# Performance work log

Hardware: AMD Instinct MI355X
Metric: run time of the kernel (lower is better)

The kernel has to match this reference:

```python
import jax, jax.numpy as jnp
import numpy as np

NX, DX, H, DO = 8192, 8, 1024, 1


def setup_inputs() -> dict:
    key = jax.random.key(0)
    ks = jax.random.split(key, 7)
    s1 = 1.0 / np.sqrt(DX)  # torch Linear default init bound
    s2 = 1.0 / np.sqrt(H)
    x = jax.random.normal(ks[0], (NX, DX), jnp.float32)
    W1 = jax.random.uniform(ks[1], (H, DX), jnp.float32, -s1, s1)
    b1 = jax.random.uniform(ks[2], (H,), jnp.float32, -s1, s1)
    W2 = jax.random.uniform(ks[3], (H, H), jnp.float32, -s2, s2)
    b2 = jax.random.uniform(ks[4], (H,), jnp.float32, -s2, s2)
    W3 = jax.random.uniform(ks[5], (DO, H), jnp.float32, -s2, s2)
    b3 = jax.random.uniform(ks[6], (DO,), jnp.float32, -s2, s2)
    return {"x": x, "W1": W1, "b1": b1, "W2": W2, "b2": b2, "W3": W3, "b3": b3}


def reference(x, W1, b1, W2, b2, W3, b3):
    # Forward: Linear -> Tanh -> Linear -> Tanh -> Linear
    z1 = jnp.tanh(x @ W1.T + b1)          # [nx, h]
    z2 = jnp.tanh(z1 @ W2.T + b2)         # [nx, h]
    y = z2 @ W3.T + b3                    # [nx, out]

    # DerivTanh(h) = 4/(e^-h + e^h)^2 = sech^2(h) = 1 - tanh(h)^2
    d1 = 1.0 - z1 * z1                    # [nx, h]
    d2 = 1.0 - z2 * z2                    # [nx, h]

    # Vectorized analytic Jacobian (original loops over each input dim k):
    # tmp_k = d2 * (W2 @ (d1 * W1[:, k]))  then  dydx_k = W3 @ tmp_k
    J = d1[:, :, None] * W1[None, :, :]                    # [nx, h, dx]
    J = d2[:, :, None] * jnp.einsum('ij,njk->nik', W2, J)  # [nx, h, dx]
    dydx = jnp.einsum('oj,njk->nok', W3, J)                # [nx, out, dx]
    # Match original list-of-dx ordering: dydx[k] has shape [nx, out]
    dydx = jnp.transpose(dydx, (2, 0, 1))                  # [dx, nx, out]
    return y, dydx
```

## Files before the change

kernel.cpp:

```cpp
#include <hip/hip_runtime.h>
#include <stdint.h>

#define NXS 8192
#define HS  1024

typedef __attribute__((ext_vector_type(8))) short short8;
typedef __attribute__((ext_vector_type(4))) float f32x4;

__device__ __forceinline__ float bf2f(uint32_t b) {
    union { uint32_t u; float f; } c; c.u = b << 16; return c.f;
}
__device__ __forceinline__ uint16_t f2bf(float f) {
    union { float f; uint32_t u; } c; c.f = f;
    return (uint16_t)((c.u + 0x7fffu + ((c.u >> 16) & 1u)) >> 16);
}
__device__ __forceinline__ void async_cp16(const void* g, void* l) {
    __builtin_amdgcn_global_load_lds(
        (const __attribute__((address_space(1))) void*)g,
        (__attribute__((address_space(3))) void*)l,
        16, 0, 0);
}

__global__ __launch_bounds__(256) void k01(
    const float* __restrict__ x, const float* __restrict__ W1,
    const float* __restrict__ b1, const float* __restrict__ W2,
    const float* __restrict__ b3, uint16_t* __restrict__ Z1,
    uint16_t* __restrict__ W2c, uint16_t* __restrict__ W2T,
    uint16_t* __restrict__ W1T, float* __restrict__ out)
{
    __shared__ float xs[8][8];
    __shared__ uint16_t tile[64][65];
    const int b = blockIdx.x;
    const int t = threadIdx.x;
    if (b < 1024) {
        const int n0 = b * 8;
        if (t < 64) xs[t >> 3][t & 7] = x[n0 * 8 + t];
        const int j = t * 4;
        float w[4][8];
#pragma unroll
        for (int c = 0; c < 4; ++c) {
            float4 w0 = *(const float4*)(W1 + (j + c) * 8);
            float4 w1 = *(const float4*)(W1 + (j + c) * 8 + 4);
            w[c][0] = w0.x; w[c][1] = w0.y; w[c][2] = w0.z; w[c][3] = w0.w;
            w[c][4] = w1.x; w[c][5] = w1.y; w[c][6] = w1.z; w[c][7] = w1.w;
        }
        float4 bb = *(const float4*)(b1 + j);
        const float bv[4] = {bb.x, bb.y, bb.z, bb.w};
        __syncthreads();
#pragma unroll
        for (int s = 0; s < 8; ++s) {
            ushort4 o;
            uint16_t* op = (uint16_t*)&o;
#pragma unroll
            for (int c = 0; c < 4; ++c) {
                float sum = bv[c];
#pragma unroll
                for (int k = 0; k < 8; ++k) sum += xs[s][k] * w[c][k];
                op[c] = f2bf(tanhf(sum));
            }
            *(ushort4*)(Z1 + (size_t)(n0 + s) * HS + j) = o;
        }
    } else if (b < 1280) {
        const int bb2 = b - 1024;
        const int bx = bb2 & 15, by = bb2 >> 4;
        const int tx = t & 63, ty = t >> 6;
#pragma unroll
        for (int rr = 0; rr < 64; rr += 4) {
            int r = ty + rr;
            uint16_t v = f2bf(W2[(size_t)(by * 64 + r) * HS + bx * 64 + tx]);
            W2c[(size_t)(by * 64 + r) * HS + bx * 64 + tx] = v;
            tile[r][tx] = v;
        }
        __syncthreads();
#pragma unroll
        for (int rr = 0; rr < 64; rr += 4)
            W2T[(size_t)(bx * 64 + ty + rr) * HS + by * 64 + tx] = tile[tx][ty + rr];
    } else if (b < 1568) {
        const int idx = (b - 1280) * 256 + t;
        out[idx] = (idx < NXS) ? b3[0] : 0.f;
    } else {
        const int idx = (b - 1568) * 256 + t;
        const int r = idx >> 10, c = idx & 1023;
        W1T[idx] = (r < 8) ? f2bf(W1[c * 8 + r]) : (uint16_t)0;
    }
}

template <int MODE>
__global__ __launch_bounds__(256, 4) void gemm_k(
    const uint16_t* __restrict__ A, const uint16_t* __restrict__ B,
    const float* __restrict__ bias, const float* __restrict__ W3,
    uint16_t* __restrict__ Out, float* __restrict__ yOut,
    const uint16_t* __restrict__ Z1, const uint16_t* __restrict__ W1T,
    float* __restrict__ dOut)
{
    __shared__ __attribute__((aligned(16))) uint16_t smem[12288];
    const int t = threadIdx.x;
    const int wave = t >> 6, lane = t & 63;
    const int lq = lane >> 4, lr = lane & 15;
    const int wm = wave >> 1, wn = wave & 1;
    const int rowBase = blockIdx.x * 64;
    const int colBase = blockIdx.y * 128;

    const int rA = t >> 2, qA = (t & 3) ^ (rA & 3);
    const int sB0 = t, sB1 = 256 + t;
    const int rB0 = sB0 >> 2, qB0 = (sB0 & 3) ^ (rB0 & 3);
    const int rB1 = sB1 >> 2, qB1 = (sB1 & 3) ^ (rB1 & 3);
    const uint16_t* gA  = A + (size_t)(rowBase + rA) * HS + qA * 8;
    const uint16_t* gB0 = B + (size_t)(colBase + rB0) * HS + qB0 * 8;
    const uint16_t* gB1 = B + (size_t)(colBase + rB1) * HS + qB1 * 8;

    f32x4 acc[2][4] = {};

    async_cp16(gA,  (char*)smem + t * 16);
    async_cp16(gB0, (char*)smem + 8192 + sB0 * 16);
    async_cp16(gB1, (char*)smem + 8192 + sB1 * 16);
    __syncthreads();

    int buf = 0;
    for (int k0 = 0; k0 < HS; k0 += 32, buf ^= 1) {
        if (k0 + 32 < HS) {
            const int ko = k0 + 32;
            async_cp16(gA + ko,  (char*)smem + (buf ^ 1) * 4096 + t * 16);
            async_cp16(gB0 + ko, (char*)smem + 8192 + (buf ^ 1) * 8192 + sB0 * 16);
            async_cp16(gB1 + ko, (char*)smem + 8192 + (buf ^ 1) * 8192 + sB1 * 16);
        }
        const short* pA = (const short*)smem + buf * 2048;
        const short* pB = (const short*)smem + 4096 + buf * 4096;
        short8 af[2], bfr[4];
#pragma unroll
        for (int ti = 0; ti < 2; ++ti) {
            int ar = wm * 32 + ti * 16 + lr;
            af[ti] = *(const short8*)(pA + ar * 32 + ((lq ^ (ar & 3)) << 3));
        }
#pragma unroll
        for (int tj = 0; tj < 4; ++tj) {
            int br = wn * 64 + tj * 16 + lr;
            bfr[tj] = *(const short8*)(pB + br * 32 + ((lq ^ (br & 3)) << 3));
        }
#pragma unroll
        for (int ti = 0; ti < 2; ++ti)
#pragma unroll
            for (int tj = 0; tj < 4; ++tj)
                acc[ti][tj] = __builtin_amdgcn_mfma_f32_16x16x32_bf16(
                    af[ti], bfr[tj], acc[ti][tj], 0, 0, 0);
        __syncthreads();
    }

    if (MODE == 0) {
        float cB[4], cW[4]; int cCol[4];
#pragma unroll
        for (int tj = 0; tj < 4; ++tj) {
            cCol[tj] = colBase + wn * 64 + tj * 16 + lr;
            cB[tj] = bias[cCol[tj]];
            cW[tj] = W3[cCol[tj]];
        }
#pragma unroll
        for (int ti = 0; ti < 2; ++ti) {
#pragma unroll
            for (int r = 0; r < 4; ++r) {
                int row = rowBase + wm * 32 + ti * 16 + lq * 4 + r;
                float ys = 0.f;
#pragma unroll
                for (int tj = 0; tj < 4; ++tj) {
                    float z2 = tanhf(acc[ti][tj][r] + cB[tj]);
                    ys += z2 * cW[tj];
                    Out[(size_t)row * HS + cCol[tj]] = f2bf((1.f - z2 * z2) * cW[tj]);
                }
                ys += __shfl_xor(ys, 1); ys += __shfl_xor(ys, 2);
                ys += __shfl_xor(ys, 4); ys += __shfl_xor(ys, 8);
                if (lr == 0) atomicAdd(&yOut[row], ys);
            }
        }
    } else {
#pragma unroll
        for (int ti = 0; ti < 2; ++ti)
#pragma unroll
            for (int r = 0; r < 4; ++r) {
                int rowl = wm * 32 + ti * 16 + lq * 4 + r;
                const size_t zrow = (size_t)(rowBase + rowl) * HS + colBase;
#pragma unroll
                for (int tj = 0; tj < 4; ++tj) {
                    int coll = wn * 64 + tj * 16 + lr;
                    float z1 = bf2f(Z1[zrow + coll]);
                    smem[rowl * 136 + coll] =
                        f2bf(acc[ti][tj][r] * (1.f - z1 * z1));
                }
            }
        __syncthreads();
        f32x4 dd = {};
#pragma unroll
        for (int kb = 0; kb < 4; ++kb) {
            short8 aF = *(const short8*)(smem + (wave * 16 + lr) * 136
                                         + kb * 32 + lq * 8);
            short8 bF = *(const short8*)(W1T + lr * HS + colBase
                                         + kb * 32 + lq * 8);
            dd = __builtin_amdgcn_mfma_f32_16x16x32_bf16(aF, bF, dd, 0, 0, 0);
        }
        if (lr < 8) {
            int row = rowBase + wave * 16 + lq * 4;
#pragma unroll
            for (int rg = 0; rg < 4; ++rg)
                atomicAdd(&dOut[(size_t)lr * NXS + row + rg], dd[rg]);
        }
    }
}

extern "C" void kernel_launch(void* const* d_in, const int* in_sizes, int n_in,
                              void* d_out, int out_size, void* d_ws, size_t ws_size,
                              hipStream_t stream) {
    (void)in_sizes; (void)n_in; (void)out_size; (void)ws_size;
    const float* x  = (const float*)d_in[0];
    const float* W1 = (const float*)d_in[1];
    const float* b1 = (const float*)d_in[2];
    const float* W2 = (const float*)d_in[3];
    const float* b2 = (const float*)d_in[4];
    const float* W3 = (const float*)d_in[5];
    const float* b3 = (const float*)d_in[6];
    float* out = (float*)d_out;

    char* ws = (char*)d_ws;
    uint16_t* Z1  = (uint16_t*)(ws);
    uint16_t* V   = (uint16_t*)(ws + (size_t)16 * 1024 * 1024);
    uint16_t* W2c = (uint16_t*)(ws + (size_t)32 * 1024 * 1024);
    uint16_t* W2T = (uint16_t*)(ws + (size_t)34 * 1024 * 1024);
    uint16_t* W1T = (uint16_t*)(ws + (size_t)36 * 1024 * 1024);

    k01<<<1632, 256, 0, stream>>>(x, W1, b1, W2, b3, Z1, W2c, W2T, W1T, out);
    gemm_k<0><<<dim3(NXS / 64, HS / 128), 256, 0, stream>>>(
        Z1, W2c, b2, W3, V, out, nullptr, nullptr, nullptr);
    gemm_k<1><<<dim3(NXS / 64, HS / 128), 256, 0, stream>>>(
        V, W2T, nullptr, nullptr, nullptr, nullptr, Z1, W1T, out + NXS);
}
```

Measured before the change: 147.2 us.

## Pre-pack W2 into MFMA fragment layout and load B operands directly into registers

The prep kernel now writes W2 and its transpose as bf16 in an MFMA-fragment-ordered layout, so each lane's 16-byte B fragment is contiguous. The GEMMs stop staging B through LDS and load these fragments straight from global memory into registers, prefetching one k-step ahead. Each wave now owns all 64 rows and 32 columns instead of a 2x2 wave grid. This removes the B tile's LDS traffic and shrinks LDS use, in exchange for more global/L2 loads of B per block, since each wave fetches its own columns.

```diff
diff --git a/kernel.cpp b/kernel.cpp
--- a/kernel.cpp
+++ b/kernel.cpp
@@ -25,13 +25,11 @@
     const float* __restrict__ x, const float* __restrict__ W1,
     const float* __restrict__ b1, const float* __restrict__ W2,
     const float* __restrict__ b3, uint16_t* __restrict__ Z1,
-    uint16_t* __restrict__ W2c, uint16_t* __restrict__ W2T,
+    uint16_t* __restrict__ Bp1, uint16_t* __restrict__ Bp2,
     uint16_t* __restrict__ W1T, float* __restrict__ out)
 {
     __shared__ float xs[8][8];
-    __shared__ uint16_t tile[64][65];
-    const int b = blockIdx.x;
-    const int t = threadIdx.x;
+    const int b = blockIdx.x, t = threadIdx.x;
     if (b < 1024) {
         const int n0 = b * 8;
         if (t < 64) xs[t >> 3][t & 7] = x[n0 * 8 + t];
@@ -60,34 +58,41 @@
             }
             *(ushort4*)(Z1 + (size_t)(n0 + s) * HS + j) = o;
         }
-    } else if (b < 1280) {
-        const int bb2 = b - 1024;
-        const int bx = bb2 & 15, by = bb2 >> 4;
-        const int tx = t & 63, ty = t >> 6;
-#pragma unroll
-        for (int rr = 0; rr < 64; rr += 4) {
-            int r = ty + rr;
-            uint16_t v = f2bf(W2[(size_t)(by * 64 + r) * HS + bx * 64 + tx]);
-            W2c[(size_t)(by * 64 + r) * HS + bx * 64 + tx] = v;
-            tile[r][tx] = v;
-        }
-        __syncthreads();
-#pragma unroll
-        for (int rr = 0; rr < 64; rr += 4)
-            W2T[(size_t)(bx * 64 + ty + rr) * HS + by * 64 + tx] = tile[tx][ty + rr];
-    } else if (b < 1568) {
-        const int idx = (b - 1280) * 256 + t;
+    } else if (b < 1536) {
+        const int tid = (b - 1024) * 256 + t;
+        const int l = tid & 63, c = (tid >> 6) & 31, g = tid >> 11;
+        const int lr = l & 15, lq = l >> 4;
+        const float* src = W2 + (size_t)(g * 16 + lr) * HS + c * 32 + lq * 8;
+        float4 a0 = *(const float4*)src;
+        float4 a1 = *(const float4*)(src + 4);
+        uint16_t o[8];
+        o[0] = f2bf(a0.x); o[1] = f2bf(a0.y); o[2] = f2bf(a0.z); o[3] = f2bf(a0.w);
+        o[4] = f2bf(a1.x); o[5] = f2bf(a1.y); o[6] = f2bf(a1.z); o[7] = f2bf(a1.w);
+        *(ushort4*)(Bp1 + (size_t)tid * 8)     = *(ushort4*)&o[0];
+        *(ushort4*)(Bp1 + (size_t)tid * 8 + 4) = *(ushort4*)&o[4];
+    } else if (b < 2048) {
+        const int tid = (b - 1536) * 256 + t;
+        const int l = tid & 63, c = (tid >> 6) & 31, g = tid >> 11;
+        const int lr = l & 15, lq = l >> 4;
+        uint16_t o[8];
+#pragma unroll
+        for (int j2 = 0; j2 < 8; ++j2)
+            o[j2] = f2bf(W2[(size_t)(c * 32 + lq * 8 + j2) * HS + g * 16 + lr]);
+        *(ushort4*)(Bp2 + (size_t)tid * 8)     = *(ushort4*)&o[0];
+        *(ushort4*)(Bp2 + (size_t)tid * 8 + 4) = *(ushort4*)&o[4];
+    } else if (b < 2336) {
+        const int idx = (b - 2048) * 256 + t;
         out[idx] = (idx < NXS) ? b3[0] : 0.f;
     } else {
-        const int idx = (b - 1568) * 256 + t;
-        const int r = idx >> 10, c = idx & 1023;
-        W1T[idx] = (r < 8) ? f2bf(W1[c * 8 + r]) : (uint16_t)0;
+        const int idx = (b - 2336) * 256 + t;
+        const int r = idx >> 10, cc = idx & 1023;
+        W1T[idx] = (r < 8) ? f2bf(W1[cc * 8 + r]) : (uint16_t)0;
     }
 }
 
 template <int MODE>
 __global__ __launch_bounds__(256, 4) void gemm_k(
-    const uint16_t* __restrict__ A, const uint16_t* __restrict__ B,
+    const uint16_t* __restrict__ A, const uint16_t* __restrict__ Bp,
     const float* __restrict__ bias, const float* __restrict__ W3,
     uint16_t* __restrict__ Out, float* __restrict__ yOut,
     const uint16_t* __restrict__ Z1, const uint16_t* __restrict__ W1T,
@@ -97,71 +102,62 @@
     const int t = threadIdx.x;
     const int wave = t >> 6, lane = t & 63;
     const int lq = lane >> 4, lr = lane & 15;
-    const int wm = wave >> 1, wn = wave & 1;
     const int rowBase = blockIdx.x * 64;
     const int colBase = blockIdx.y * 128;
 
     const int rA = t >> 2, qA = (t & 3) ^ (rA & 3);
-    const int sB0 = t, sB1 = 256 + t;
-    const int rB0 = sB0 >> 2, qB0 = (sB0 & 3) ^ (rB0 & 3);
-    const int rB1 = sB1 >> 2, qB1 = (sB1 & 3) ^ (rB1 & 3);
-    const uint16_t* gA  = A + (size_t)(rowBase + rA) * HS + qA * 8;
-    const uint16_t* gB0 = B + (size_t)(colBase + rB0) * HS + qB0 * 8;
-    const uint16_t* gB1 = B + (size_t)(colBase + rB1) * HS + qB1 * 8;
-
-    f32x4 acc[2][4] = {};
-
-    async_cp16(gA,  (char*)smem + t * 16);
-    async_cp16(gB0, (char*)smem + 8192 + sB0 * 16);
-    async_cp16(gB1, (char*)smem + 8192 + sB1 * 16);
+    const uint16_t* gA = A + (size_t)(rowBase + rA) * HS + qA * 8;
+
+    const uint16_t* pB0 = Bp + ((size_t)(colBase >> 4) + wave * 2) * 16384 + (size_t)lane * 8;
+    const uint16_t* pB1 = pB0 + 16384;
+
+    f32x4 acc[4][2] = {};
+
+    async_cp16(gA, (char*)smem + t * 16);
+    short8 b0 = *(const short8*)pB0;
+    short8 b1 = *(const short8*)pB1;
     __syncthreads();
 
     int buf = 0;
-    for (int k0 = 0; k0 < HS; k0 += 32, buf ^= 1) {
-        if (k0 + 32 < HS) {
-            const int ko = k0 + 32;
-            async_cp16(gA + ko,  (char*)smem + (buf ^ 1) * 4096 + t * 16);
-            async_cp16(gB0 + ko, (char*)smem + 8192 + (buf ^ 1) * 8192 + sB0 * 16);
-            async_cp16(gB1 + ko, (char*)smem + 8192 + (buf ^ 1) * 8192 + sB1 * 16);
+    for (int c = 0; c < 32; ++c, buf ^= 1) {
+        short8 b0n = b0, b1n = b1;
+        if (c < 31) {
+            async_cp16(gA + (c + 1) * 32, (char*)smem + (buf ^ 1) * 4096 + t * 16);
+            b0n = *(const short8*)(pB0 + (c + 1) * 512);
+            b1n = *(const short8*)(pB1 + (c + 1) * 512);
         }
         const short* pA = (const short*)smem + buf * 2048;
-        const short* pB = (const short*)smem + 4096 + buf * 4096;
-        short8 af[2], bfr[4];
-#pragma unroll
-        for (int ti = 0; ti < 2; ++ti) {
-            int ar = wm * 32 + ti * 16 + lr;
+        short8 af[4];
+#pragma unroll
+        for (int ti = 0; ti < 4; ++ti) {
+            int ar = ti * 16 + lr;
             af[ti] = *(const short8*)(pA + ar * 32 + ((lq ^ (ar & 3)) << 3));
         }
 #pragma unroll
-        for (int tj = 0; tj < 4; ++tj) {
-            int br = wn * 64 + tj * 16 + lr;
-            bfr[tj] = *(const short8*)(pB + br * 32 + ((lq ^ (br & 3)) << 3));
-        }
-#pragma unroll
-        for (int ti = 0; ti < 2; ++ti)
-#pragma unroll
-            for (int tj = 0; tj < 4; ++tj)
-                acc[ti][tj] = __builtin_amdgcn_mfma_f32_16x16x32_bf16(
-                    af[ti], bfr[tj], acc[ti][tj], 0, 0, 0);
+        for (int ti = 0; ti < 4; ++ti) {
+            acc[ti][0] = __builtin_amdgcn_mfma_f32_16x16x32_bf16(af[ti], b0, acc[ti][0], 0, 0, 0);
+            acc[ti][1] = __builtin_amdgcn_mfma_f32_16x16x32_bf16(af[ti], b1, acc[ti][1], 0, 0, 0);
+        }
         __syncthreads();
+        b0 = b0n; b1 = b1n;
     }
 
     if (MODE == 0) {
-        float cB[4], cW[4]; int cCol[4];
-#pragma unroll
-        for (int tj = 0; tj < 4; ++tj) {
-            cCol[tj] = colBase + wn * 64 + tj * 16 + lr;
+        float cB[2], cW[2]; int cCol[2];
+#pragma unroll
+        for (int tj = 0; tj < 2; ++tj) {
+            cCol[tj] = colBase + wave * 32 + tj * 16 + lr;
             cB[tj] = bias[cCol[tj]];
             cW[tj] = W3[cCol[tj]];
         }
 #pragma unroll
-        for (int ti = 0; ti < 2; ++ti) {
+        for (int ti = 0; ti < 4; ++ti) {
 #pragma unroll
             for (int r = 0; r < 4; ++r) {
-                int row = rowBase + wm * 32 + ti * 16 + lq * 4 + r;
+                int row = rowBase + ti * 16 + lq * 4 + r;
                 float ys = 0.f;
 #pragma unroll
-                for (int tj = 0; tj < 4; ++tj) {
+                for (int tj = 0; tj < 2; ++tj) {
                     float z2 = tanhf(acc[ti][tj][r] + cB[tj]);
                     ys += z2 * cW[tj];
                     Out[(size_t)row * HS + cCol[tj]] = f2bf((1.f - z2 * z2) * cW[tj]);
@@ -173,14 +169,14 @@
         }
     } else {
 #pragma unroll
-        for (int ti = 0; ti < 2; ++ti)
+        for (int ti = 0; ti < 4; ++ti)
 #pragma unroll
             for (int r = 0; r < 4; ++r) {
-                int rowl = wm * 32 + ti * 16 + lq * 4 + r;
+                int rowl = ti * 16 + lq * 4 + r;
                 const size_t zrow = (size_t)(rowBase + rowl) * HS + colBase;
 #pragma unroll
-                for (int tj = 0; tj < 4; ++tj) {
-                    int coll = wn * 64 + tj * 16 + lr;
+                for (int tj = 0; tj < 2; ++tj) {
+                    int coll = wave * 32 + tj * 16 + lr;
                     float z1 = bf2f(Z1[zrow + coll]);
                     smem[rowl * 136 + coll] =
                         f2bf(acc[ti][tj][r] * (1.f - z1 * z1));
@@ -221,13 +217,13 @@
     char* ws = (char*)d_ws;
     uint16_t* Z1  = (uint16_t*)(ws);
     uint16_t* V   = (uint16_t*)(ws + (size_t)16 * 1024 * 1024);
-    uint16_t* W2c = (uint16_t*)(ws + (size_t)32 * 1024 * 1024);
-    uint16_t* W2T = (uint16_t*)(ws + (size_t)34 * 1024 * 1024);
+    uint16_t* Bp1 = (uint16_t*)(ws + (size_t)32 * 1024 * 1024);
+    uint16_t* Bp2 = (uint16_t*)(ws + (size_t)34 * 1024 * 1024);
     uint16_t* W1T = (uint16_t*)(ws + (size_t)36 * 1024 * 1024);
 
-    k01<<<1632, 256, 0, stream>>>(x, W1, b1, W2, b3, Z1, W2c, W2T, W1T, out);
+    k01<<<2400, 256, 0, stream>>>(x, W1, b1, W2, b3, Z1, Bp1, Bp2, W1T, out);
     gemm_k<0><<<dim3(NXS / 64, HS / 128), 256, 0, stream>>>(
-        Z1, W2c, b2, W3, V, out, nullptr, nullptr, nullptr);
+        Z1, Bp1, b2, W3, V, out, nullptr, nullptr, nullptr);
     gemm_k<1><<<dim3(NXS / 64, HS / 128), 256, 0, stream>>>(
-        V, W2T, nullptr, nullptr, nullptr, nullptr, Z1, W1T, out + NXS);
-}
+        V, Bp2, nullptr, nullptr, nullptr, nullptr, Z1, W1T, out + NXS);
+}
```

New measurement: 136.8 us. -7.1%, faster.
